# Kernel tuning notes

Hardware: AMD Instinct MI355X
Metric: run time of the kernel (lower is better)

Reference implementation:

```python
import jax, jax.numpy as jnp
import numpy as np

PS = 16          # patch_size
D = 768          # embed_dim (= conv_output_channels)
CIN = 8          # in_chans
HID = 128        # hypernet hidden width
WSIZE = D * PS * PS  # per-channel conv weight size (out=D, in=1, PSxPS)


def setup_inputs() -> dict:
    key = jax.random.key(0)
    ks = jax.random.split(key, 7)
    B, H, W = 32, 224, 224
    x = jax.random.normal(ks[0], (B, CIN, H, W), dtype=jnp.float32)
    channels = jax.random.randint(ks[1], (B, CIN), 0, CIN)
    # learned params; linears stored as [in, out] (math identical to torch x @ W.T + b)
    channel_embed = 0.02 * jax.random.normal(ks[2], (CIN, D), dtype=jnp.float32)
    fc1_w = jax.random.normal(ks[3], (D, HID), dtype=jnp.float32) / np.sqrt(D)
    fc1_b = jnp.zeros((HID,), dtype=jnp.float32)
    fc2_w = jax.random.normal(ks[4], (HID, WSIZE + D), dtype=jnp.float32) / np.sqrt(HID)
    fc2_b = jnp.zeros((WSIZE + D,), dtype=jnp.float32)
    return {"x": x, "channels": channels, "channel_embed": channel_embed,
            "fc1_w": fc1_w, "fc1_b": fc1_b, "fc2_w": fc2_w, "fc2_b": fc2_b}


def reference(x, channels, channel_embed, fc1_w, fc1_b, fc2_w, fc2_b):
    B, Cin, H, W = x.shape
    Hp, Wp = H // PS, W // PS
    # cur_channel_embed is computed in the original forward but never used
    _ = channel_embed[channels]
    # hypernetwork, batched over all channels (replaces the python loop)
    h = jax.nn.relu(channel_embed @ fc1_w + fc1_b)         # [Cin, 128]
    y = jnp.tanh(h @ fc2_w + fc2_b)                        # [Cin, WSIZE + D]
    wts = y[:, :WSIZE].reshape(Cin, D, PS, PS)             # per-channel conv kernels
    bias = y[:, WSIZE:]                                    # [Cin, D]
    # stride==kernel conv2d == non-overlapping patch matmul
    patches = x.reshape(B, Cin, Hp, PS, Wp, PS)
    out = jnp.einsum('bchpwq,cdpq->bchwd', patches, wts) + bias[None, :, None, None, :]
    # torch: stack(dim=2)->[B,D,Cin,Hp,Wp], flatten(2), transpose(1,2) => token order (c,h,w)
    return out.reshape(B, Cin * Hp * Wp, D)
```

## Files before the change

kernel.cpp:

```cpp
#include <hip/hip_runtime.h>
#include <hip/hip_bf16.h>

#define CIN 8
#define IMG 224
#define PS 16
#define HP 14
#define D_ 768
#define HID 128
#define MPT 196
#define K_ 256
#define WSIZE 196608
#define NJ 197376
#define XN (32 * CIN * IMG * IMG)

typedef __bf16 bf16x8 __attribute__((ext_vector_type(8)));
typedef float f32x4 __attribute__((ext_vector_type(4)));

static __device__ __forceinline__ ushort f2bf(float f) {
  union { float f; unsigned int u; } x; x.f = f;
  unsigned int r = x.u + 0x7fffu + ((x.u >> 16) & 1u);
  return (ushort)(r >> 16);
}

static __device__ __forceinline__ void gload16(const void* g, void* l) {
  __builtin_amdgcn_global_load_lds(
      (const __attribute__((address_space(1))) unsigned int*)(uintptr_t)g,
      (__attribute__((address_space(3))) unsigned int*)(uintptr_t)l, 16, 0, 0);
}

__global__ __launch_bounds__(512) void k1_fc1(const float* __restrict__ ce,
                                              const float* __restrict__ w1,
                                              const float* __restrict__ b1,
                                              float* __restrict__ ht) {
  __shared__ float sh[3][HID];
  int c = blockIdx.x;
  int t = threadIdx.x;
  int i = t & 127, ksp = t >> 7;
  const float* cev = ce + c * D_ + ksp * 192;
  const float* wp = w1 + (size_t)(ksp * 192) * HID + i;
  float acc = 0.f;
#pragma unroll 8
  for (int d = 0; d < 192; ++d) acc = fmaf(cev[d], wp[(size_t)d * HID], acc);
  if (ksp) sh[ksp - 1][i] = acc;
  __syncthreads();
  if (ksp == 0) {
    float s = b1[i] + acc + sh[0][i] + sh[1][i] + sh[2][i];
    ht[i * CIN + c] = fmaxf(s, 0.f);
  }
}

__global__ __launch_bounds__(256) void k2_fused(
    const float* __restrict__ ht, const float* __restrict__ w2,
    const float* __restrict__ b2, const float* __restrict__ x,
    ushort* __restrict__ wbf, float* __restrict__ biasOut,
    ushort* __restrict__ xbf, int nCol) {
  int bid = blockIdx.x;
  int t = threadIdx.x;
  if (bid >= nCol) {
    int u = (bid - nCol) * 256 + t;
    int stride = (gridDim.x - nCol) * 256;
    const float4* xv = (const float4*)x;
    for (int v = u; v < XN / 8; v += stride) {
      float4 f0 = xv[v * 2], f1 = xv[v * 2 + 1];
      union { ushort s[8]; uint4 q; } pk;
      pk.s[0] = f2bf(f0.x); pk.s[1] = f2bf(f0.y); pk.s[2] = f2bf(f0.z); pk.s[3] = f2bf(f0.w);
      pk.s[4] = f2bf(f1.x); pk.s[5] = f2bf(f1.y); pk.s[6] = f2bf(f1.z); pk.s[7] = f2bf(f1.w);
      *(uint4*)(xbf + (size_t)v * 8) = pk.q;
    }
    return;
  }
  int j = bid * 256 + t;
  const float* wp = w2 + j;
  const float4* ht4 = (const float4*)ht;
  float4 a0 = {0, 0, 0, 0}, a1 = {0, 0, 0, 0};
#pragma unroll 8
  for (int i = 0; i < HID; ++i) {
    float wv = wp[(size_t)i * NJ];
    float4 hA = ht4[i * 2], hB = ht4[i * 2 + 1];
    a0.x = fmaf(hA.x, wv, a0.x); a0.y = fmaf(hA.y, wv, a0.y);
    a0.z = fmaf(hA.z, wv, a0.z); a0.w = fmaf(hA.w, wv, a0.w);
    a1.x = fmaf(hB.x, wv, a1.x); a1.y = fmaf(hB.y, wv, a1.y);
    a1.z = fmaf(hB.z, wv, a1.z); a1.w = fmaf(hB.w, wv, a1.w);
  }
  float bb = b2[j];
  if (j < WSIZE) {
    wbf[(size_t)0 * WSIZE + j] = f2bf(tanhf(a0.x + bb));
    wbf[(size_t)1 * WSIZE + j] = f2bf(tanhf(a0.y + bb));
    wbf[(size_t)2 * WSIZE + j] = f2bf(tanhf(a0.z + bb));
    wbf[(size_t)3 * WSIZE + j] = f2bf(tanhf(a0.w + bb));
    wbf[(size_t)4 * WSIZE + j] = f2bf(tanhf(a1.x + bb));
    wbf[(size_t)5 * WSIZE + j] = f2bf(tanhf(a1.y + bb));
    wbf[(size_t)6 * WSIZE + j] = f2bf(tanhf(a1.z + bb));
    wbf[(size_t)7 * WSIZE + j] = f2bf(tanhf(a1.w + bb));
  } else {
    int jb = j - WSIZE;
    biasOut[0 * D_ + jb] = tanhf(a0.x + bb);
    biasOut[1 * D_ + jb] = tanhf(a0.y + bb);
    biasOut[2 * D_ + jb] = tanhf(a0.z + bb);
    biasOut[3 * D_ + jb] = tanhf(a0.w + bb);
    biasOut[4 * D_ + jb] = tanhf(a1.x + bb);
    biasOut[5 * D_ + jb] = tanhf(a1.y + bb);
    biasOut[6 * D_ + jb] = tanhf(a1.z + bb);
    biasOut[7 * D_ + jb] = tanhf(a1.w + bb);
  }
}

#define BK 64

template <bool PRE>
__global__ __launch_bounds__(256, 2) void k3_gemm(
    const float* __restrict__ x, const ushort* __restrict__ xbf,
    const ushort* __restrict__ wbf, const float* __restrict__ bias,
    float* __restrict__ out) {
  constexpr int LDKE = PRE ? 64 : 72;
  __shared__ ushort As[128 * LDKE];
  __shared__ ushort Bs[128 * LDKE];

  int bid = blockIdx.x;
  int c = bid & 7;
  int rem = bid >> 3;
  int mt = rem / 6;
  int nt = rem - mt * 6;
  int m0 = mt * 128, n0 = nt * 128;

  int t = threadIdx.x;
  int lane = t & 63;
  int w = t >> 6;
  int wr = w >> 1, wc = w & 1;

  const ushort* wsrc = wbf + (size_t)c * WSIZE + (size_t)n0 * K_;

  f32x4 acc[4][4] = {};

  if constexpr (PRE) {
    int subrow = lane >> 3;
    int pq = (lane & 7) ^ subrow;
    const ushort* aptr[4];
    const ushort* bptr[4];
#pragma unroll
    for (int j = 0; j < 4; ++j) {
      int g = w * 4 + j;
      int m_l = g * 8 + subrow;
      int m = m0 + m_l;
      int b = m / MPT;
      int hw = m - b * MPT;
      int hp = hw / HP;
      int wp = hw - hp * HP;
      aptr[j] = xbf + (((size_t)(b * CIN + c) * IMG + hp * PS) * IMG + wp * PS)
              + (pq >> 1) * IMG + (pq & 1) * 8;
      bptr[j] = wsrc + (g * 8 + subrow) * K_ + pq * 8;
    }

    for (int ks = 0; ks < 4; ++ks) {
      __syncthreads();
#pragma unroll
      for (int j = 0; j < 4; ++j) {
        int g = w * 4 + j;
        gload16(aptr[j] + ks * (4 * IMG), &As[g * 512]);
        gload16(bptr[j] + ks * BK, &Bs[g * 512]);
      }
      __syncthreads();
#pragma unroll
      for (int kk = 0; kk < BK; kk += 32) {
        bf16x8 af[4], bfr[4];
#pragma unroll
        for (int mi = 0; mi < 4; ++mi) {
          int row = wr * 64 + mi * 16 + (lane & 15);
          af[mi] = *(const bf16x8*)&As[row * 64 +
                     ((kk + (lane >> 4) * 8) ^ ((row & 7) << 3))];
        }
#pragma unroll
        for (int ni = 0; ni < 4; ++ni) {
          int row = wc * 64 + ni * 16 + (lane & 15);
          bfr[ni] = *(const bf16x8*)&Bs[row * 64 +
                      ((kk + (lane >> 4) * 8) ^ ((row & 7) << 3))];
        }
#pragma unroll
        for (int mi = 0; mi < 4; ++mi)
#pragma unroll
          for (int ni = 0; ni < 4; ++ni)
            acc[mi][ni] = __builtin_amdgcn_mfma_f32_16x16x32_bf16(af[mi], bfr[ni], acc[mi][ni], 0, 0, 0);
      }
    }
  } else {
    int m_l = t & 127;
    int pgrp = t >> 7;
    int m = m0 + m_l;
    int b = m / MPT;
    int hw = m - b * MPT;
    int hp = hw / HP;
    int wp = hw - hp * HP;
    const float* xrow0 = x + (((size_t)(b * CIN + c) * IMG + hp * PS) * IMG + wp * PS);

    for (int ks = 0; ks < 4; ++ks) {
      __syncthreads();
#pragma unroll
      for (int s = 0; s < 2; ++s) {
        int pl = s * 2 + pgrp;
        const float* src = xrow0 + (ks * 4 + pl) * IMG;
        float4 f0 = *(const float4*)(src + 0);
        float4 f1 = *(const float4*)(src + 4);
        float4 f2 = *(const float4*)(src + 8);
        float4 f3 = *(const float4*)(src + 12);
        union { ushort u[16]; uint4 v[2]; } pk;
        pk.u[0]  = f2bf(f0.x); pk.u[1]  = f2bf(f0.y); pk.u[2]  = f2bf(f0.z); pk.u[3]  = f2bf(f0.w);
        pk.u[4]  = f2bf(f1.x); pk.u[5]  = f2bf(f1.y); pk.u[6]  = f2bf(f1.z); pk.u[7]  = f2bf(f1.w);
        pk.u[8]  = f2bf(f2.x); pk.u[9]  = f2bf(f2.y); pk.u[10] = f2bf(f2.z); pk.u[11] = f2bf(f2.w);
        pk.u[12] = f2bf(f3.x); pk.u[13] = f2bf(f3.y); pk.u[14] = f2bf(f3.z); pk.u[15] = f2bf(f3.w);
        uint4* dst = (uint4*)&As[m_l * LDKE + pl * 16];
        dst[0] = pk.v[0];
        dst[1] = pk.v[1];
      }
#pragma unroll
      for (int i2 = 0; i2 < 4; ++i2) {
        int cg = t + i2 * 256;
        int n_l = cg >> 3, part = cg & 7;
        *(uint4*)&Bs[n_l * LDKE + part * 8] =
            *(const uint4*)(wsrc + n_l * K_ + ks * BK + part * 8);
      }
      __syncthreads();
#pragma unroll
      for (int kk = 0; kk < BK; kk += 32) {
        bf16x8 af[4], bfr[4];
#pragma unroll
        for (int mi = 0; mi < 4; ++mi)
          af[mi] = *(const bf16x8*)&As[(wr * 64 + mi * 16 + (lane & 15)) * LDKE + kk + (lane >> 4) * 8];
#pragma unroll
        for (int ni = 0; ni < 4; ++ni)
          bfr[ni] = *(const bf16x8*)&Bs[(wc * 64 + ni * 16 + (lane & 15)) * LDKE + kk + (lane >> 4) * 8];
#pragma unroll
        for (int mi = 0; mi < 4; ++mi)
#pragma unroll
          for (int ni = 0; ni < 4; ++ni)
            acc[mi][ni] = __builtin_amdgcn_mfma_f32_16x16x32_bf16(af[mi], bfr[ni], acc[mi][ni], 0, 0, 0);
      }
    }
  }

  int col_l = lane & 15;
  int rowg = lane >> 4;
  float bv[4];
#pragma unroll
  for (int ni = 0; ni < 4; ++ni)
    bv[ni] = bias[c * D_ + n0 + wc * 64 + ni * 16 + col_l];
#pragma unroll
  for (int mi = 0; mi < 4; ++mi) {
#pragma unroll
    for (int r = 0; r < 4; ++r) {
      int mrow = m0 + wr * 64 + mi * 16 + rowg * 4 + r;
      int b2 = mrow / MPT;
      int hw2 = mrow - b2 * MPT;
      float* op = out + ((size_t)b2 * (CIN * MPT) + c * MPT + hw2) * D_ + n0 + wc * 64 + col_l;
#pragma unroll
      for (int ni = 0; ni < 4; ++ni)
        op[ni * 16] = acc[mi][ni][r] + bv[ni];
    }
  }
}

extern "C" void kernel_launch(void* const* d_in, const int* in_sizes, int n_in,
                              void* d_out, int out_size, void* d_ws, size_t ws_size,
                              hipStream_t stream) {
  const float* x  = (const float*)d_in[0];
  const float* ce = (const float*)d_in[2];
  const float* w1 = (const float*)d_in[3];
  const float* b1 = (const float*)d_in[4];
  const float* w2 = (const float*)d_in[5];
  const float* b2 = (const float*)d_in[6];
  float* out = (float*)d_out;

  char* ws = (char*)d_ws;
  float*  ht      = (float*)ws;
  float*  biasOut = (float*)(ws + 4096);
  ushort* wbf     = (ushort*)(ws + 4096 + 24576);
  ushort* xbf     = (ushort*)(ws + 4096 + 24576 + 3145728);
  const size_t NEED = 4096 + 24576 + 3145728 + (size_t)XN * 2;

  bool pre = ws_size >= NEED;
  int nCol = NJ / 256;
  int nConv = pre ? 512 : 0;

  k1_fc1<<<dim3(CIN), dim3(512), 0, stream>>>(ce, w1, b1, ht);
  k2_fused<<<dim3(nCol + nConv), dim3(256), 0, stream>>>(ht, w2, b2, x, wbf, biasOut, xbf, nCol);
  if (pre)
    k3_gemm<true><<<dim3(8 * 49 * 6), dim3(256), 0, stream>>>(x, xbf, wbf, biasOut, out);
  else
    k3_gemm<false><<<dim3(8 * 49 * 6), dim3(256), 0, stream>>>(x, xbf, wbf, biasOut, out);
}
```

Before: 95.60 us.

## Drop x bf16 pre-pass; load fp32 A fragments directly to registers in GEMM

Removes the separate pass that converted the whole input image to bf16 in workspace. The GEMM now loads fp32 patch rows straight into registers, converts them to MFMA A fragments, and skips LDS staging for A. It also loads the full 128x256 B tile into swizzled LDS once, so only one barrier is needed instead of a per-k-step sync loop. In exchange, 64KB of LDS per block may limit occupancy, and each 6 N-tile blocks re-read x in fp32 from global memory without LDS sharing.

```diff
diff --git a/kernel.cpp b/kernel.cpp
--- a/kernel.cpp
+++ b/kernel.cpp
@@ -11,7 +11,6 @@
 #define K_ 256
 #define WSIZE 196608
 #define NJ 197376
-#define XN (32 * CIN * IMG * IMG)
 
 typedef __bf16 bf16x8 __attribute__((ext_vector_type(8)));
 typedef float f32x4 __attribute__((ext_vector_type(4)));
@@ -49,27 +48,12 @@
   }
 }
 
-__global__ __launch_bounds__(256) void k2_fused(
+__global__ __launch_bounds__(256) void k2_fc2(
     const float* __restrict__ ht, const float* __restrict__ w2,
-    const float* __restrict__ b2, const float* __restrict__ x,
-    ushort* __restrict__ wbf, float* __restrict__ biasOut,
-    ushort* __restrict__ xbf, int nCol) {
-  int bid = blockIdx.x;
+    const float* __restrict__ b2, ushort* __restrict__ wbf,
+    float* __restrict__ biasOut) {
   int t = threadIdx.x;
-  if (bid >= nCol) {
-    int u = (bid - nCol) * 256 + t;
-    int stride = (gridDim.x - nCol) * 256;
-    const float4* xv = (const float4*)x;
-    for (int v = u; v < XN / 8; v += stride) {
-      float4 f0 = xv[v * 2], f1 = xv[v * 2 + 1];
-      union { ushort s[8]; uint4 q; } pk;
-      pk.s[0] = f2bf(f0.x); pk.s[1] = f2bf(f0.y); pk.s[2] = f2bf(f0.z); pk.s[3] = f2bf(f0.w);
-      pk.s[4] = f2bf(f1.x); pk.s[5] = f2bf(f1.y); pk.s[6] = f2bf(f1.z); pk.s[7] = f2bf(f1.w);
-      *(uint4*)(xbf + (size_t)v * 8) = pk.q;
-    }
-    return;
-  }
-  int j = bid * 256 + t;
+  int j = blockIdx.x * 256 + t;
   const float* wp = w2 + j;
   const float4* ht4 = (const float4*)ht;
   float4 a0 = {0, 0, 0, 0}, a1 = {0, 0, 0, 0};
@@ -105,16 +89,10 @@
   }
 }
 
-#define BK 64
-
-template <bool PRE>
 __global__ __launch_bounds__(256, 2) void k3_gemm(
-    const float* __restrict__ x, const ushort* __restrict__ xbf,
-    const ushort* __restrict__ wbf, const float* __restrict__ bias,
-    float* __restrict__ out) {
-  constexpr int LDKE = PRE ? 64 : 72;
-  __shared__ ushort As[128 * LDKE];
-  __shared__ ushort Bs[128 * LDKE];
+    const float* __restrict__ x, const ushort* __restrict__ wbf,
+    const float* __restrict__ bias, float* __restrict__ out) {
+  __shared__ ushort Bs[128 * 256];
 
   int bid = blockIdx.x;
   int c = bid & 7;
@@ -127,118 +105,77 @@
   int lane = t & 63;
   int w = t >> 6;
   int wr = w >> 1, wc = w & 1;
+  int rB = lane & 15;
+  int h = lane >> 4;
 
   const ushort* wsrc = wbf + (size_t)c * WSIZE + (size_t)n0 * K_;
 
-  f32x4 acc[4][4] = {};
-
-  if constexpr (PRE) {
-    int subrow = lane >> 3;
-    int pq = (lane & 7) ^ subrow;
-    const ushort* aptr[4];
-    const ushort* bptr[4];
-#pragma unroll
-    for (int j = 0; j < 4; ++j) {
-      int g = w * 4 + j;
-      int m_l = g * 8 + subrow;
-      int m = m0 + m_l;
-      int b = m / MPT;
-      int hw = m - b * MPT;
-      int hp = hw / HP;
-      int wp = hw - hp * HP;
-      aptr[j] = xbf + (((size_t)(b * CIN + c) * IMG + hp * PS) * IMG + wp * PS)
-              + (pq >> 1) * IMG + (pq & 1) * 8;
-      bptr[j] = wsrc + (g * 8 + subrow) * K_ + pq * 8;
-    }
-
-    for (int ks = 0; ks < 4; ++ks) {
-      __syncthreads();
-#pragma unroll
-      for (int j = 0; j < 4; ++j) {
-        int g = w * 4 + j;
-        gload16(aptr[j] + ks * (4 * IMG), &As[g * 512]);
-        gload16(bptr[j] + ks * BK, &Bs[g * 512]);
-      }
-      __syncthreads();
-#pragma unroll
-      for (int kk = 0; kk < BK; kk += 32) {
-        bf16x8 af[4], bfr[4];
-#pragma unroll
-        for (int mi = 0; mi < 4; ++mi) {
-          int row = wr * 64 + mi * 16 + (lane & 15);
-          af[mi] = *(const bf16x8*)&As[row * 64 +
-                     ((kk + (lane >> 4) * 8) ^ ((row & 7) << 3))];
-        }
-#pragma unroll
-        for (int ni = 0; ni < 4; ++ni) {
-          int row = wc * 64 + ni * 16 + (lane & 15);
-          bfr[ni] = *(const bf16x8*)&Bs[row * 64 +
-                      ((kk + (lane >> 4) * 8) ^ ((row & 7) << 3))];
-        }
-#pragma unroll
-        for (int mi = 0; mi < 4; ++mi)
-#pragma unroll
-          for (int ni = 0; ni < 4; ++ni)
-            acc[mi][ni] = __builtin_amdgcn_mfma_f32_16x16x32_bf16(af[mi], bfr[ni], acc[mi][ni], 0, 0, 0);
-      }
-    }
-  } else {
-    int m_l = t & 127;
-    int pgrp = t >> 7;
-    int m = m0 + m_l;
-    int b = m / MPT;
-    int hw = m - b * MPT;
+  int hb = (h >> 1) * IMG + (h & 1) * 8;
+  const float* ap[4];
+#pragma unroll
+  for (int mi = 0; mi < 4; ++mi) {
+    int rowA = m0 + wr * 64 + mi * 16 + rB;
+    int b = rowA / MPT;
+    int hw = rowA - b * MPT;
     int hp = hw / HP;
     int wp = hw - hp * HP;
-    const float* xrow0 = x + (((size_t)(b * CIN + c) * IMG + hp * PS) * IMG + wp * PS);
-
-    for (int ks = 0; ks < 4; ++ks) {
-      __syncthreads();
-#pragma unroll
-      for (int s = 0; s < 2; ++s) {
-        int pl = s * 2 + pgrp;
-        const float* src = xrow0 + (ks * 4 + pl) * IMG;
-        float4 f0 = *(const float4*)(src + 0);
-        float4 f1 = *(const float4*)(src + 4);
-        float4 f2 = *(const float4*)(src + 8);
-        float4 f3 = *(const float4*)(src + 12);
-        union { ushort u[16]; uint4 v[2]; } pk;
-        pk.u[0]  = f2bf(f0.x); pk.u[1]  = f2bf(f0.y); pk.u[2]  = f2bf(f0.z); pk.u[3]  = f2bf(f0.w);
-        pk.u[4]  = f2bf(f1.x); pk.u[5]  = f2bf(f1.y); pk.u[6]  = f2bf(f1.z); pk.u[7]  = f2bf(f1.w);
-        pk.u[8]  = f2bf(f2.x); pk.u[9]  = f2bf(f2.y); pk.u[10] = f2bf(f2.z); pk.u[11] = f2bf(f2.w);
-        pk.u[12] = f2bf(f3.x); pk.u[13] = f2bf(f3.y); pk.u[14] = f2bf(f3.z); pk.u[15] = f2bf(f3.w);
-        uint4* dst = (uint4*)&As[m_l * LDKE + pl * 16];
-        dst[0] = pk.v[0];
-        dst[1] = pk.v[1];
+    ap[mi] = x + ((size_t)(b * CIN + c) * IMG + hp * PS) * IMG + wp * PS + hb;
+  }
+
+  float4 pf0[4], pf1[4];
+#pragma unroll
+  for (int mi = 0; mi < 4; ++mi) {
+    pf0[mi] = *(const float4*)(ap[mi]);
+    pf1[mi] = *(const float4*)(ap[mi] + 4);
+  }
+
+#pragma unroll
+  for (int i = 0; i < 16; ++i) {
+    int g = i * 256 + t;
+    int row = g >> 5;
+    int q = t & 31;
+    int p = (q & 16) | ((q ^ row) & 15);
+    gload16(wsrc + row * K_ + p * 8, &Bs[i * 2048 + w * 512]);
+  }
+  __syncthreads();
+
+  f32x4 acc[4][4] = {};
+
+#pragma unroll
+  for (int ks = 0; ks < 4; ++ks) {
+#pragma unroll
+    for (int kc = 0; kc < 2; ++kc) {
+      bf16x8 af[4], bq[4];
+#pragma unroll
+      for (int mi = 0; mi < 4; ++mi) {
+        float4 f0, f1;
+        if (ks == 0 && kc == 0) { f0 = pf0[mi]; f1 = pf1[mi]; }
+        else {
+          const float* s = ap[mi] + (ks * 4 + kc * 2) * IMG;
+          f0 = *(const float4*)s;
+          f1 = *(const float4*)(s + 4);
+        }
+        union { ushort u[8]; bf16x8 v; } pk;
+        pk.u[0] = f2bf(f0.x); pk.u[1] = f2bf(f0.y); pk.u[2] = f2bf(f0.z); pk.u[3] = f2bf(f0.w);
+        pk.u[4] = f2bf(f1.x); pk.u[5] = f2bf(f1.y); pk.u[6] = f2bf(f1.z); pk.u[7] = f2bf(f1.w);
+        af[mi] = pk.v;
       }
-#pragma unroll
-      for (int i2 = 0; i2 < 4; ++i2) {
-        int cg = t + i2 * 256;
-        int n_l = cg >> 3, part = cg & 7;
-        *(uint4*)&Bs[n_l * LDKE + part * 8] =
-            *(const uint4*)(wsrc + n_l * K_ + ks * BK + part * 8);
-      }
-      __syncthreads();
-#pragma unroll
-      for (int kk = 0; kk < BK; kk += 32) {
-        bf16x8 af[4], bfr[4];
-#pragma unroll
-        for (int mi = 0; mi < 4; ++mi)
-          af[mi] = *(const bf16x8*)&As[(wr * 64 + mi * 16 + (lane & 15)) * LDKE + kk + (lane >> 4) * 8];
+      int pc = ks * 8 + kc * 4;
+      int tq = ((pc & 15) + h) ^ rB;
+      int qoff = ((pc & 16) << 3) + tq * 8;
+#pragma unroll
+      for (int ni = 0; ni < 4; ++ni)
+        bq[ni] = *(const bf16x8*)&Bs[(wc * 64 + ni * 16 + rB) * 256 + qoff];
+#pragma unroll
+      for (int mi = 0; mi < 4; ++mi)
 #pragma unroll
         for (int ni = 0; ni < 4; ++ni)
-          bfr[ni] = *(const bf16x8*)&Bs[(wc * 64 + ni * 16 + (lane & 15)) * LDKE + kk + (lane >> 4) * 8];
-#pragma unroll
-        for (int mi = 0; mi < 4; ++mi)
-#pragma unroll
-          for (int ni = 0; ni < 4; ++ni)
-            acc[mi][ni] = __builtin_amdgcn_mfma_f32_16x16x32_bf16(af[mi], bfr[ni], acc[mi][ni], 0, 0, 0);
-      }
+          acc[mi][ni] = __builtin_amdgcn_mfma_f32_16x16x32_bf16(af[mi], bq[ni], acc[mi][ni], 0, 0, 0);
     }
   }
 
-  int col_l = lane & 15;
-  int rowg = lane >> 4;
+  int col_l = rB;
+  int rowg = h;
   float bv[4];
 #pragma unroll
   for (int ni = 0; ni < 4; ++ni)
@@ -273,17 +210,8 @@
   float*  ht      = (float*)ws;
   float*  biasOut = (float*)(ws + 4096);
   ushort* wbf     = (ushort*)(ws + 4096 + 24576);
-  ushort* xbf     = (ushort*)(ws + 4096 + 24576 + 3145728);
-  const size_t NEED = 4096 + 24576 + 3145728 + (size_t)XN * 2;
-
-  bool pre = ws_size >= NEED;
-  int nCol = NJ / 256;
-  int nConv = pre ? 512 : 0;
 
   k1_fc1<<<dim3(CIN), dim3(512), 0, stream>>>(ce, w1, b1, ht);
-  k2_fused<<<dim3(nCol + nConv), dim3(256), 0, stream>>>(ht, w2, b2, x, wbf, biasOut, xbf, nCol);
-  if (pre)
-    k3_gemm<true><<<dim3(8 * 49 * 6), dim3(256), 0, stream>>>(x, xbf, wbf, biasOut, out);
-  else
-    k3_gemm<false><<<dim3(8 * 49 * 6), dim3(256), 0, stream>>>(x, xbf, wbf, biasOut, out);
-}
+  k2_fc2<<<dim3(NJ / 256), dim3(256), 0, stream>>>(ht, w2, b2, wbf, biasOut);
+  k3_gemm<<<dim3(8 * 49 * 6), dim3(256), 0, stream>>>(x, wbf, biasOut, out);
+}
```

Measured after the change: 147.7 us. +54.5%, slower.
